# Kernel tuning notes

Hardware: AMD Instinct MI355X
Metric: run time of the kernel (lower is better)

The kernel has to match this reference:

```python
import jax, jax.numpy as jnp
import numpy as np

N_U, N_I, E = 500000, 50000, 1000000
H, C = 4, 32  # heads, per-head channels


def _seg_softmax(e, dst, n_dst):
    # e: [E, H] edge scores, softmax over edges sharing the same destination
    m = jax.ops.segment_max(e, dst, num_segments=n_dst)
    ex = jnp.exp(e - m[dst])
    s = jax.ops.segment_sum(ex, dst, num_segments=n_dst)
    return ex / (s[dst] + 1e-16)


def _gatv2(xl, xr, src, dst, att, bias, n_dst, edge_feat=None):
    # GATv2 bipartite message passing (PyG semantics, no self-loops for bipartite).
    # xl: [N_src,H,C] transformed source, xr: [N_dst,H,C] transformed destination
    h = xl[src] + xr[dst]                      # [E,H,C] gather + add
    if edge_feat is not None:
        h = h + edge_feat                      # [E,H,C]
    e = jnp.sum(jax.nn.leaky_relu(h, 0.2) * att, axis=-1)   # [E,H]
    alpha = _seg_softmax(e, dst, n_dst)                      # [E,H]
    out = jax.ops.segment_sum(alpha[..., None] * xl[src], dst, num_segments=n_dst)
    return out.reshape(n_dst, H * C) + bias    # concat heads + bias


def setup_inputs() -> dict:
    key = jax.random.key(0)
    ks = iter(jax.random.split(key, 32))
    p = lambda *s: jax.random.normal(next(ks), s, dtype=jnp.float32) * 0.05
    inp = {
        "customer_x": jax.random.normal(next(ks), (N_U, 101), dtype=jnp.float32),
        "fund_x": jax.random.normal(next(ks), (N_I, 1), dtype=jnp.float32),
        "edge_attr": jax.random.uniform(next(ks), (E, 3), dtype=jnp.float32),
        "edge_src": jax.random.randint(next(ks), (E,), 0, N_U),
        "edge_dst": jax.random.randint(next(ks), (E,), 0, N_I),
        # input projections
        "user_W": p(101, 32), "user_b": jnp.zeros((32,), jnp.float32),
        "item_W": p(1, 32),   "item_b": jnp.zeros((32,), jnp.float32),
        # conv1: GATv2Conv((32,32), 32, heads=4, edge_dim=3)
        "c1_Wl": p(32, H * C), "c1_bl": jnp.zeros((H * C,), jnp.float32),
        "c1_Wr": p(32, H * C), "c1_br": jnp.zeros((H * C,), jnp.float32),
        "c1_We": p(3, H * C),
        "c1_att": p(H, C), "c1_bias": jnp.zeros((H * C,), jnp.float32),
        # conv2: GATv2Conv((128,32), 32, heads=4), called without edge_attr
        "c2_Wl": p(H * C, H * C), "c2_bl": jnp.zeros((H * C,), jnp.float32),
        "c2_Wr": p(32, H * C),    "c2_br": jnp.zeros((H * C,), jnp.float32),
        "c2_att": p(H, C), "c2_bias": jnp.zeros((H * C,), jnp.float32),
        # classifier MLP: 128 -> 64 -> 1
        "cls_W1": p(128, 64), "cls_b1": jnp.zeros((64,), jnp.float32),
        "cls_W2": p(64, 1),   "cls_b2": jnp.zeros((1,), jnp.float32),
    }
    return inp


def reference(customer_x, fund_x, edge_attr, edge_src, edge_dst,
              user_W, user_b, item_W, item_b,
              c1_Wl, c1_bl, c1_Wr, c1_br, c1_We, c1_att, c1_bias,
              c2_Wl, c2_bl, c2_Wr, c2_br, c2_att, c2_bias,
              cls_W1, cls_b1, cls_W2, cls_b2):
    user_x = customer_x @ user_W + user_b            # [N_U,32]
    item_x = fund_x @ item_W + item_b                # [N_I,32]
    # conv1: customer -> fund (dst = fund)
    xl1 = (user_x @ c1_Wl + c1_bl).reshape(N_U, H, C)
    xr1 = (item_x @ c1_Wr + c1_br).reshape(N_I, H, C)
    ef1 = (edge_attr @ c1_We).reshape(E, H, C)
    item_h = jax.nn.relu(_gatv2(xl1, xr1, edge_src, edge_dst, c1_att, c1_bias, N_I, ef1))
    # conv2: fund -> customer (edge_index flipped, no edge_attr)
    xl2 = (item_h @ c2_Wl + c2_bl).reshape(N_I, H, C)
    xr2 = (user_x @ c2_Wr + c2_br).reshape(N_U, H, C)
    user_h = _gatv2(xl2, xr2, edge_dst, edge_src, c2_att, c2_bias, N_U)  # [N_U,128]
    # anomaly classifier
    hid = jax.nn.relu(user_h @ cls_W1 + cls_b1)
    scores = jax.nn.sigmoid(hid @ cls_W2 + cls_b2)   # [N_U,1]
    return scores
```

## Files before the change

kernel.cpp:

```cpp
#include <hip/hip_runtime.h>
#include <cstdint>
#include <cstddef>

#define NU 500000
#define NI 50000
#define NE 1000000
#define HC 128
#define NH 4

typedef __attribute__((ext_vector_type(8))) short bf16x8;
typedef __attribute__((ext_vector_type(4))) float f32x4;

union frag_u { bf16x8 v; unsigned int u[4]; };

__device__ __forceinline__ unsigned int pack_bf2(float x, float y) {
    unsigned int r;
    asm("v_cvt_pk_bf16_f32 %0, %1, %2" : "=v"(r) : "v"(x), "v"(y));
    return r;
}
__device__ __forceinline__ float2 unpack_bf2(unsigned int v) {
    return make_float2(__uint_as_float(v << 16),
                       __uint_as_float(v & 0xffff0000u));
}
__device__ __forceinline__ unsigned short pack_bf1(float x) {
    unsigned int b = __float_as_uint(x);
    b += 0x7fffu + ((b >> 16) & 1u);
    return (unsigned short)(b >> 16);
}

__device__ __forceinline__ float head_reduce(float p) {
    p += __shfl_xor(p, 8, 16);
    p += __shfl_xor(p, 4, 16);
    p += __shfl_xor(p, 2, 16);
    p += __shfl_xor(p, 1, 16);
    return p;
}

__global__ void wprep(const float* __restrict__ user_W, const float* __restrict__ user_b,
                      const float* __restrict__ c1_Wl, const float* __restrict__ c1_bl,
                      const float* __restrict__ c2_Wr, const float* __restrict__ c2_br,
                      const float* __restrict__ c2_Wl, unsigned short* __restrict__ Bp)
{
    const int t = blockIdx.x * 256 + threadIdx.x;
    const int mat = t >> 14;
    const int k = (t >> 7) & 127;
    const int n = t & 127;
    float val = 0.f;
    if (mat == 2) {
        val = c2_Wl[k * 128 + n];
    } else {
        const float* W2 = mat ? c2_Wr : c1_Wl;
        if (k < 101) {
            for (int q = 0; q < 32; ++q) val = fmaf(user_W[k * 32 + q], W2[q * 128 + n], val);
        } else if (k == 101) {
            for (int q = 0; q < 32; ++q) val = fmaf(user_b[q], W2[q * 128 + n], val);
            val += (mat ? c2_br : c1_bl)[n];
        }
    }
    const int fi = (mat * 8 + (n >> 4)) * 4 + (k >> 5);
    const int lane_ = (n & 15) + ((k >> 3) & 3) * 16;
    Bp[(size_t)fi * 512 + lane_ * 8 + (k & 7)] = pack_bf1(val);
}

__global__ void w1prep(const float* __restrict__ W1, unsigned short* __restrict__ Bp1)
{
    const int t = blockIdx.x * 256 + threadIdx.x;
    const int k = t >> 6;
    const int n = t & 63;
    const float val = W1[k * 64 + n];
    const int fi = (n >> 4) * 4 + (k >> 5);
    const int lane_ = (n & 15) + ((k >> 3) & 3) * 16;
    Bp1[(size_t)fi * 512 + lane_ * 8 + (k & 7)] = pack_bf1(val);
}

__global__ void wvbb_prep(const float* __restrict__ item_W, const float* __restrict__ item_b,
                          const float* __restrict__ c1_Wr, const float* __restrict__ c1_br,
                          float* __restrict__ wvbb)
{
    const int j = threadIdx.x;
    if (j >= 128) return;
    float wv = 0.f, bb = 0.f;
    for (int q = 0; q < 32; ++q) {
        wv = fmaf(item_W[q], c1_Wr[q * 128 + j], wv);
        bb = fmaf(item_b[q], c1_Wr[q * 128 + j], bb);
    }
    wvbb[j] = wv;
    wvbb[128 + j] = bb + c1_br[j];
}

__global__ __launch_bounds__(256)
void mfma_user(const float* __restrict__ cx, const unsigned short* __restrict__ Bp,
               unsigned short* __restrict__ outL, unsigned short* __restrict__ outR, int M)
{
    __shared__ float xs[64 * 108];

    const int tid = threadIdx.x;
    const int lane = tid & 63;
    const int wid = tid >> 6;
    const int rowblk = blockIdx.x * 64;
    const int rows = min(64, M - rowblk);

    const float* src = cx + (size_t)rowblk * 101;
    const int total = rows * 101;
    for (int i = tid; i < total; i += 256) {
        const int r = i / 101;
        const int c = i - r * 101;
        xs[r * 108 + c] = src[i];
    }
    __syncthreads();

    const int rowbase = wid * 16;
    if (rowbase >= rows) return;
    const int row = lane & 15;
    const int chunk = lane >> 4;
    const float* rowp = xs + (rowbase + row) * 108;

    frag_u a[4];
    #pragma unroll
    for (int ks = 0; ks < 3; ++ks) {
        const int kb = ks * 32 + chunk * 8;
        const float4 p = *(const float4*)(rowp + kb);
        const float4 q = *(const float4*)(rowp + kb + 4);
        a[ks].u[0] = pack_bf2(p.x, p.y);
        a[ks].u[1] = pack_bf2(p.z, p.w);
        a[ks].u[2] = pack_bf2(q.x, q.y);
        a[ks].u[3] = pack_bf2(q.z, q.w);
    }
    {
        float v0 = 0.f, v1 = 0.f, v2 = 0.f, v3 = 0.f, v4 = 0.f, v5 = 0.f;
        if (chunk == 0) {
            const float4 p = *(const float4*)(rowp + 96);
            v0 = p.x; v1 = p.y; v2 = p.z; v3 = p.w;
            v4 = rowp[100];
            v5 = 1.0f;
        }
        a[3].u[0] = pack_bf2(v0, v1);
        a[3].u[1] = pack_bf2(v2, v3);
        a[3].u[2] = pack_bf2(v4, v5);
        a[3].u[3] = 0u;
    }

    unsigned short* xpo = (unsigned short*)(xs + (size_t)wid * 16 * 108);

    const bf16x8* bfr = (const bf16x8*)Bp;
    #pragma unroll
    for (int mat = 0; mat < 2; ++mat) {
        unsigned short* outp = mat ? outR : outL;
        #pragma unroll
        for (int nf = 0; nf < 8; ++nf) {
            f32x4 acc = {0.f, 0.f, 0.f, 0.f};
            const int fi = (mat * 8 + nf) * 4;
            acc = __builtin_amdgcn_mfma_f32_16x16x32_bf16(a[0].v, bfr[(fi + 0) * 64 + lane], acc, 0, 0, 0);
            acc = __builtin_amdgcn_mfma_f32_16x16x32_bf16(a[1].v, bfr[(fi + 1) * 64 + lane], acc, 0, 0, 0);
            acc = __builtin_amdgcn_mfma_f32_16x16x32_bf16(a[2].v, bfr[(fi + 2) * 64 + lane], acc, 0, 0, 0);
            acc = __builtin_amdgcn_mfma_f32_16x16x32_bf16(a[3].v, bfr[(fi + 3) * 64 + lane], acc, 0, 0, 0);
            const int col = nf * 16 + row;
            #pragma unroll
            for (int j = 0; j < 4; ++j)
                xpo[(chunk * 4 + j) * 140 + col] = pack_bf1(acc[j]);
        }
        #pragma unroll
        for (int i = 0; i < 4; ++i) {
            const int r = i * 4 + chunk;
            const bf16x8 v = *(const bf16x8*)&xpo[r * 140 + row * 8];
            *(bf16x8*)(outp + (size_t)(rowblk + rowbase + r) * 128 + row * 8) = v;
        }
    }
}

__global__ __launch_bounds__(256)
void mfma_xl2(const float* __restrict__ X, const unsigned short* __restrict__ Bp,
              const float* __restrict__ bias, unsigned short* __restrict__ outp, int M)
{
    const int lane = threadIdx.x & 63;
    const int wt = (blockIdx.x * blockDim.x + threadIdx.x) >> 6;
    const int rowbase = wt * 16;
    if (rowbase >= M) return;
    const int chunk = lane >> 4;
    const float* rowp = X + (size_t)(rowbase + (lane & 15)) * 128;

    frag_u a[4];
    #pragma unroll
    for (int ks = 0; ks < 4; ++ks) {
        const int kb = ks * 32 + chunk * 8;
        const float4 p = *(const float4*)(rowp + kb);
        const float4 q = *(const float4*)(rowp + kb + 4);
        a[ks].u[0] = pack_bf2(p.x, p.y);
        a[ks].u[1] = pack_bf2(p.z, p.w);
        a[ks].u[2] = pack_bf2(q.x, q.y);
        a[ks].u[3] = pack_bf2(q.z, q.w);
    }

    const bf16x8* bfr = (const bf16x8*)Bp;
    #pragma unroll
    for (int nf = 0; nf < 8; ++nf) {
        f32x4 acc = {0.f, 0.f, 0.f, 0.f};
        const int fi = (16 + nf) * 4;
        acc = __builtin_amdgcn_mfma_f32_16x16x32_bf16(a[0].v, bfr[(fi + 0) * 64 + lane], acc, 0, 0, 0);
        acc = __builtin_amdgcn_mfma_f32_16x16x32_bf16(a[1].v, bfr[(fi + 1) * 64 + lane], acc, 0, 0, 0);
        acc = __builtin_amdgcn_mfma_f32_16x16x32_bf16(a[2].v, bfr[(fi + 2) * 64 + lane], acc, 0, 0, 0);
        acc = __builtin_amdgcn_mfma_f32_16x16x32_bf16(a[3].v, bfr[(fi + 3) * 64 + lane], acc, 0, 0, 0);
        const int col = nf * 16 + (lane & 15);
        const float bv = bias[col];
        #pragma unroll
        for (int j = 0; j < 4; ++j)
            outp[(size_t)(rowbase + chunk * 4 + j) * 128 + col] = pack_bf1(acc[j] + bv);
    }
}

__global__ void hist_rank(const int* __restrict__ src, const int* __restrict__ dst,
                          int* __restrict__ cntU, int* __restrict__ cntI,
                          int* __restrict__ rankU, int* __restrict__ rankI, int E)
{
    for (int i = blockIdx.x * blockDim.x + threadIdx.x; i < E;
         i += gridDim.x * blockDim.x) {
        rankU[i] = atomicAdd(&cntU[src[i]], 1);
        rankI[i] = atomicAdd(&cntI[dst[i]], 1);
    }
}

__global__ void scan_blocks(const int* __restrict__ in, int* __restrict__ out,
                            int* __restrict__ blockSums, int n)
{
    __shared__ int lds[256];
    const int tid = threadIdx.x;
    const int base = blockIdx.x * 1024 + tid * 4;
    int v[4];
    #pragma unroll
    for (int j = 0; j < 4; ++j) { int idx = base + j; v[j] = (idx < n) ? in[idx] : 0; }
    int t = v[0] + v[1] + v[2] + v[3];
    lds[tid] = t;
    __syncthreads();
    for (int off = 1; off < 256; off <<= 1) {
        int x = (tid >= off) ? lds[tid - off] : 0;
        __syncthreads();
        lds[tid] += x;
        __syncthreads();
    }
    int excl = lds[tid] - t;
    if (tid == 255 && blockSums) blockSums[blockIdx.x] = lds[255];
    int run = excl;
    #pragma unroll
    for (int j = 0; j < 4; ++j) {
        int idx = base + j;
        if (idx < n) out[idx] = run;
        run += v[j];
    }
}

__global__ void scan_add(int* __restrict__ out, const int* __restrict__ bss, int n)
{
    const int add = bss[blockIdx.x];
    const int base = blockIdx.x * 1024 + threadIdx.x * 4;
    #pragma unroll
    for (int j = 0; j < 4; ++j) { int idx = base + j; if (idx < n) out[idx] += add; }
}

__global__ void scatter_ranked(const int* __restrict__ src, const int* __restrict__ dst,
                               const float* __restrict__ eattr,
                               const int* __restrict__ offU, const int* __restrict__ offI,
                               const int* __restrict__ rankU, const int* __restrict__ rankI,
                               int* __restrict__ sFund, uint4* __restrict__ sE1, int E)
{
    for (int i = blockIdx.x * blockDim.x + threadIdx.x; i < E;
         i += gridDim.x * blockDim.x) {
        const int s = src[i];
        const int d = dst[i];
        const float a0 = eattr[3 * (size_t)i];
        const float a1 = eattr[3 * (size_t)i + 1];
        const float a2 = eattr[3 * (size_t)i + 2];
        const int p1 = offI[d] + rankI[i];
        const int p2 = offU[s] + rankU[i];
        sE1[p1] = make_uint4((unsigned int)s, __float_as_uint(a0),
                             __float_as_uint(a1), __float_as_uint(a2));
        sFund[p2] = d;
    }
}

__device__ __forceinline__ void conv1_edge(uint4 e, unsigned int vbits, float2 vr,
                                           float2 av, float2 w0, float2 w1, float2 w2,
                                           float& acc0, float& acc1, float& s)
{
    const float2 vl = unpack_bf2(vbits);
    const float e0 = __uint_as_float(e.y);
    const float e1 = __uint_as_float(e.z);
    const float e2 = __uint_as_float(e.w);
    float h0 = vl.x + vr.x + e0 * w0.x + e1 * w1.x + e2 * w2.x;
    float h1 = vl.y + vr.y + e0 * w0.y + e1 * w1.y + e2 * w2.y;
    h0 = h0 > 0.f ? h0 : 0.2f * h0;
    h1 = h1 > 0.f ? h1 : 0.2f * h1;
    const float p = head_reduce(h0 * av.x + h1 * av.y);
    const float ex = __expf(p);
    acc0 = fmaf(ex, vl.x, acc0);
    acc1 = fmaf(ex, vl.y, acc1);
    s += ex;
}

__global__ void conv1_fused(const unsigned int* __restrict__ xl,
                            const float* __restrict__ fund_x,
                            const float* __restrict__ wvbb,
                            const int* __restrict__ offI, const int* __restrict__ cnt,
                            const uint4* __restrict__ sE,
                            const float* __restrict__ We, const float* __restrict__ att,
                            const float* __restrict__ bias,
                            float* __restrict__ outF, int ndst)
{
    const int tid = threadIdx.x;
    const int lane = tid & 63;
    const int wid = tid >> 6;
    const int d = blockIdx.x * 4 + wid;
    if (d >= ndst) return;

    const int ch = lane * 2;
    const float2 av = *(const float2*)(att + ch);
    const float2 w0 = *(const float2*)(We + ch);
    const float2 w1 = *(const float2*)(We + HC + ch);
    const float2 w2 = *(const float2*)(We + 2 * HC + ch);
    const float2 bv = *(const float2*)(bias + ch);

    const float fx = fund_x[d];
    const float2 wv = *(const float2*)(wvbb + ch);
    const float2 bb = *(const float2*)(wvbb + 128 + ch);
    const float2 vr = make_float2(fmaf(fx, wv.x, bb.x), fmaf(fx, wv.y, bb.y));

    const int start = offI[d];
    const int end = start + cnt[d];

    float acc0 = 0.f, acc1 = 0.f, s = 0.f;
    int pos = start;
    for (; pos + 8 <= end; pos += 8) {
        uint4 e[8];
        unsigned int v[8];
        #pragma unroll
        for (int j = 0; j < 8; ++j) e[j] = sE[pos + j];
        #pragma unroll
        for (int j = 0; j < 8; ++j) v[j] = xl[(size_t)e[j].x * 64 + lane];
        #pragma unroll
        for (int j = 0; j < 8; ++j)
            conv1_edge(e[j], v[j], vr, av, w0, w1, w2, acc0, acc1, s);
    }
    for (; pos + 4 <= end; pos += 4) {
        uint4 e[4];
        unsigned int v[4];
        #pragma unroll
        for (int j = 0; j < 4; ++j) e[j] = sE[pos + j];
        #pragma unroll
        for (int j = 0; j < 4; ++j) v[j] = xl[(size_t)e[j].x * 64 + lane];
        #pragma unroll
        for (int j = 0; j < 4; ++j)
            conv1_edge(e[j], v[j], vr, av, w0, w1, w2, acc0, acc1, s);
    }
    for (; pos < end; ++pos) {
        const uint4 e = sE[pos];
        const unsigned int v = xl[(size_t)e.x * 64 + lane];
        conv1_edge(e, v, vr, av, w0, w1, w2, acc0, acc1, s);
    }
    const float inv = 1.f / (s + 1e-16f);
    const float o0 = fmaxf(acc0 * inv + bv.x, 0.f);
    const float o1 = fmaxf(acc1 * inv + bv.y, 0.f);
    *(float2*)(outF + (size_t)d * HC + ch) = make_float2(o0, o1);
}

__device__ __forceinline__ void conv2_edge(unsigned int vbits, float2 vr, float2 av,
                                           float& acc0, float& acc1, float& s)
{
    const float2 vl = unpack_bf2(vbits);
    float h0 = vl.x + vr.x;
    float h1 = vl.y + vr.y;
    h0 = h0 > 0.f ? h0 : 0.2f * h0;
    h1 = h1 > 0.f ? h1 : 0.2f * h1;
    const float p = head_reduce(h0 * av.x + h1 * av.y);
    const float ex = __expf(p);
    acc0 = fmaf(ex, vl.x, acc0);
    acc1 = fmaf(ex, vl.y, acc1);
    s += ex;
}

__global__ __launch_bounds__(256)
void conv2_cls(const unsigned int* __restrict__ xl2,
               const unsigned int* __restrict__ xr2,
               const int* __restrict__ offU, const int* __restrict__ cnt,
               const int* __restrict__ sFund,
               const float* __restrict__ att, const float* __restrict__ cbias,
               const unsigned short* __restrict__ Bp1,
               const float* __restrict__ b1, const float* __restrict__ W2,
               const float* __restrict__ b2,
               float* __restrict__ out, int nusr)
{
    __shared__ unsigned short xs[4][16][136];

    const int lane = threadIdx.x & 63;
    const int wid = threadIdx.x >> 6;
    const int wt = (blockIdx.x * blockDim.x + threadIdx.x) >> 6;
    const int u0 = wt * 16;
    if (u0 >= nusr) return;

    const int ch = lane * 2;
    const float2 av = *(const float2*)(att + ch);
    const float2 bv = *(const float2*)(cbias + ch);

    int so = 0, ctv = 0;
    if (lane < 16) {
        so = offU[u0 + lane];
        ctv = cnt[u0 + lane];
    }
    const int eo = so + ctv;
    const int S = __builtin_amdgcn_readlane(so, 0);
    const int E = __builtin_amdgcn_readlane(eo, 15);

    int u = 0;
    int end_u = __builtin_amdgcn_readlane(eo, 0);
    unsigned int vrb_next = xr2[(size_t)(u0 + 1) * 64 + lane];
    float2 vr = unpack_bf2(xr2[(size_t)u0 * 64 + lane]);
    float acc0 = 0.f, acc1 = 0.f, s = 0.f;

    #define FINALIZE() {                                                        \
        const float inv = 1.f / (s + 1e-16f);                                   \
        *(unsigned int*)&xs[wid][u][ch] = pack_bf2(acc0 * inv + bv.x,           \
                                                   acc1 * inv + bv.y);          \
        acc0 = acc1 = s = 0.f;                                                  \
        ++u;                                                                    \
        if (u < 16) {                                                           \
            end_u = __builtin_amdgcn_readlane(eo, u);                           \
            vr = unpack_bf2(vrb_next);                                          \
            if (u + 1 < 16) vrb_next = xr2[(size_t)(u0 + u + 1) * 64 + lane];   \
        }                                                                       \
    }

    int pos = S;
    while (pos < E) {
        const int f0 = sFund[pos];
        const int f1 = (pos + 1 < E) ? sFund[pos + 1] : f0;
        const int f2 = (pos + 2 < E) ? sFund[pos + 2] : f0;
        const int f3 = (pos + 3 < E) ? sFund[pos + 3] : f0;
        const unsigned int v0 = xl2[(size_t)f0 * 64 + lane];
        const unsigned int v1 = xl2[(size_t)f1 * 64 + lane];
        const unsigned int v2 = xl2[(size_t)f2 * 64 + lane];
        const unsigned int v3 = xl2[(size_t)f3 * 64 + lane];

        while (pos == end_u) FINALIZE();
        conv2_edge(v0, vr, av, acc0, acc1, s);
        if (pos + 1 < E) {
            while (pos + 1 == end_u) FINALIZE();
            conv2_edge(v1, vr, av, acc0, acc1, s);
        }
        if (pos + 2 < E) {
            while (pos + 2 == end_u) FINALIZE();
            conv2_edge(v2, vr, av, acc0, acc1, s);
        }
        if (pos + 3 < E) {
            while (pos + 3 == end_u) FINALIZE();
            conv2_edge(v3, vr, av, acc0, acc1, s);
        }
        pos += 4;
    }
    while (u < 16) FINALIZE();
    #undef FINALIZE

    const int row = lane & 15;
    const int chunk = lane >> 4;
    bf16x8 a[4];
    #pragma unroll
    for (int ks = 0; ks < 4; ++ks)
        a[ks] = *(const bf16x8*)&xs[wid][row][ks * 32 + chunk * 8];

    const bf16x8* bfr = (const bf16x8*)Bp1;
    float racc[4] = {0.f, 0.f, 0.f, 0.f};
    #pragma unroll
    for (int g = 0; g < 4; ++g) {
        f32x4 acc = {0.f, 0.f, 0.f, 0.f};
        const int fi = g * 4;
        acc = __builtin_amdgcn_mfma_f32_16x16x32_bf16(a[0], bfr[(fi + 0) * 64 + lane], acc, 0, 0, 0);
        acc = __builtin_amdgcn_mfma_f32_16x16x32_bf16(a[1], bfr[(fi + 1) * 64 + lane], acc, 0, 0, 0);
        acc = __builtin_amdgcn_mfma_f32_16x16x32_bf16(a[2], bfr[(fi + 2) * 64 + lane], acc, 0, 0, 0);
        acc = __builtin_amdgcn_mfma_f32_16x16x32_bf16(a[3], bfr[(fi + 3) * 64 + lane], acc, 0, 0, 0);
        const int col = g * 16 + row;
        const float b1v = b1[col];
        const float w2v = W2[col];
        #pragma unroll
        for (int j = 0; j < 4; ++j)
            racc[j] = fmaf(fmaxf(acc[j] + b1v, 0.f), w2v, racc[j]);
    }
    #pragma unroll
    for (int j = 0; j < 4; ++j) {
        racc[j] += __shfl_xor(racc[j], 1, 16);
        racc[j] += __shfl_xor(racc[j], 2, 16);
        racc[j] += __shfl_xor(racc[j], 4, 16);
        racc[j] += __shfl_xor(racc[j], 8, 16);
    }
    if (row == 0) {
        const float b2v = b2[0];
        #pragma unroll
        for (int j = 0; j < 4; ++j) {
            const int r = u0 + chunk * 4 + j;
            if (r < nusr) out[r] = 1.f / (1.f + expf(-(racc[j] + b2v)));
        }
    }
}

extern "C" void kernel_launch(void* const* d_in, const int* in_sizes, int n_in,
                              void* d_out, int out_size, void* d_ws, size_t ws_size,
                              hipStream_t stream)
{
    const float* customer_x = (const float*)d_in[0];
    const float* fund_x     = (const float*)d_in[1];
    const float* edge_attr  = (const float*)d_in[2];
    const int*   edge_src   = (const int*)d_in[3];
    const int*   edge_dst   = (const int*)d_in[4];
    const float* user_W = (const float*)d_in[5];
    const float* user_b = (const float*)d_in[6];
    const float* item_W = (const float*)d_in[7];
    const float* item_b = (const float*)d_in[8];
    const float* c1_Wl  = (const float*)d_in[9];
    const float* c1_bl  = (const float*)d_in[10];
    const float* c1_Wr  = (const float*)d_in[11];
    const float* c1_br  = (const float*)d_in[12];
    const float* c1_We  = (const float*)d_in[13];
    const float* c1_att = (const float*)d_in[14];
    const float* c1_bias= (const float*)d_in[15];
    const float* c2_Wl  = (const float*)d_in[16];
    const float* c2_bl  = (const float*)d_in[17];
    const float* c2_Wr  = (const float*)d_in[18];
    const float* c2_br  = (const float*)d_in[19];
    const float* c2_att = (const float*)d_in[20];
    const float* c2_bias= (const float*)d_in[21];
    const float* cls_W1 = (const float*)d_in[22];
    const float* cls_b1 = (const float*)d_in[23];
    const float* cls_W2 = (const float*)d_in[24];
    const float* cls_b2 = (const float*)d_in[25];
    float* out = (float*)d_out;

    float* ws = (float*)d_ws;
    size_t off = 0;
    unsigned short* B1 = (unsigned short*)(ws + off); off += (size_t)NU * 64;
    unsigned short* B2 = (unsigned short*)(ws + off); off += (size_t)NU * 64;
    float* F = ws + off; off += (size_t)NI * HC;
    unsigned short* G = (unsigned short*)(ws + off); off += (size_t)NI * 64;
    int* cnt1  = (int*)(ws + off); off += NI;
    int* off1  = (int*)(ws + off); off += NI;
    int* cnt2  = (int*)(ws + off); off += NU;
    int* off2  = (int*)(ws + off); off += NU;
    int* bs    = (int*)(ws + off); off += 1024;
    int* bss   = (int*)(ws + off); off += 1024;
    uint4* sE1 = (uint4*)(ws + off); off += (size_t)NE * 4;
    int* sFund = (int*)(ws + off); off += NE;
    int* rankU = (int*)(ws + off); off += NE;
    int* rankI = (int*)(ws + off); off += NE;
    unsigned short* Bp = (unsigned short*)(ws + off); off += 12288 + 256;
    unsigned short* Bp1 = (unsigned short*)(ws + off); off += 4096 + 256;
    float* wvbb = ws + off; off += 256;

    hipMemsetAsync(cnt1, 0, NI * sizeof(int), stream);
    hipMemsetAsync(cnt2, 0, NU * sizeof(int), stream);

    hist_rank<<<1024, 256, 0, stream>>>(edge_src, edge_dst, cnt2, cnt1,
                                        rankU, rankI, NE);
    const int nb1 = (NI + 1023) / 1024;
    const int nb2 = (NU + 1023) / 1024;
    scan_blocks<<<nb1, 256, 0, stream>>>(cnt1, off1, bs, NI);
    scan_blocks<<<1,   256, 0, stream>>>(bs, bss, nullptr, nb1);
    scan_add<<<nb1, 256, 0, stream>>>(off1, bss, NI);
    scan_blocks<<<nb2, 256, 0, stream>>>(cnt2, off2, bs, NU);
    scan_blocks<<<1,   256, 0, stream>>>(bs, bss, nullptr, nb2);
    scan_add<<<nb2, 256, 0, stream>>>(off2, bss, NU);
    scatter_ranked<<<2048, 256, 0, stream>>>(edge_src, edge_dst, edge_attr,
                                             off2, off1, rankU, rankI,
                                             sFund, sE1, NE);

    wprep<<<192, 256, 0, stream>>>(user_W, user_b, c1_Wl, c1_bl,
                                   c2_Wr, c2_br, c2_Wl, Bp);
    w1prep<<<32, 256, 0, stream>>>(cls_W1, Bp1);
    wvbb_prep<<<1, 128, 0, stream>>>(item_W, item_b, c1_Wr, c1_br, wvbb);

    mfma_user<<<(NU + 63) / 64, 256, 0, stream>>>(customer_x, Bp, B1, B2, NU);

    conv1_fused<<<NI / 4, 256, 0, stream>>>((const unsigned int*)B1, fund_x, wvbb,
                                            off1, cnt1, sE1,
                                            c1_We, c1_att, c1_bias, F, NI);

    mfma_xl2<<<(NI / 16 + 3) / 4, 256, 0, stream>>>(F, Bp, c2_bl, G, NI);

    const int waves2 = (NU + 15) / 16;
    conv2_cls<<<(waves2 + 3) / 4, 256, 0, stream>>>(
        (const unsigned int*)G, (const unsigned int*)B2, off2, cnt2, sFund,
        c2_att, c2_bias, Bp1, cls_b1, cls_W2, cls_b2, out, NU);
}
```

Measured before the change: 537.3 us.

## Fuse edge scatter into user MFMA kernel via extra blocks for overlap

Removes the standalone scatter_ranked launch and appends 2048 extra blocks to the user-projection MFMA kernel, which perform the edge scatter. The aim is to overlap the memory-bound scatter with the projection and save one kernel launch and drain. In exchange, the scatter blocks are scheduled after the projection blocks, so overlap may be limited and both parts compete for memory bandwidth. The combined kernel also keeps the 27 KB LDS allocation for the scatter blocks, which can lower occupancy for them.

```diff
diff --git a/kernel.cpp b/kernel.cpp
--- a/kernel.cpp
+++ b/kernel.cpp
@@ -89,10 +89,33 @@
 }
 
 __global__ __launch_bounds__(256)
-void mfma_user(const float* __restrict__ cx, const unsigned short* __restrict__ Bp,
-               unsigned short* __restrict__ outL, unsigned short* __restrict__ outR, int M)
+void mfma_user_scatter(const float* __restrict__ cx, const unsigned short* __restrict__ Bp,
+                       unsigned short* __restrict__ outL, unsigned short* __restrict__ outR,
+                       int M, int nub,
+                       const int* __restrict__ src, const int* __restrict__ dst,
+                       const float* __restrict__ eattr,
+                       const int* __restrict__ offU, const int* __restrict__ offI,
+                       const int* __restrict__ rankU, const int* __restrict__ rankI,
+                       int* __restrict__ sFund, uint4* __restrict__ sE1, int E, int nscat)
 {
     __shared__ float xs[64 * 108];
+
+    if (blockIdx.x >= nub) {
+        const int bid = blockIdx.x - nub;
+        for (int i = bid * 256 + threadIdx.x; i < E; i += nscat * 256) {
+            const int s = src[i];
+            const int d = dst[i];
+            const float a0 = eattr[3 * (size_t)i];
+            const float a1 = eattr[3 * (size_t)i + 1];
+            const float a2 = eattr[3 * (size_t)i + 2];
+            const int p1 = offI[d] + rankI[i];
+            const int p2 = offU[s] + rankU[i];
+            sE1[p1] = make_uint4((unsigned int)s, __float_as_uint(a0),
+                                 __float_as_uint(a1), __float_as_uint(a2));
+            sFund[p2] = d;
+        }
+        return;
+    }
 
     const int tid = threadIdx.x;
     const int lane = tid & 63;
@@ -100,12 +123,12 @@
     const int rowblk = blockIdx.x * 64;
     const int rows = min(64, M - rowblk);
 
-    const float* src = cx + (size_t)rowblk * 101;
+    const float* srcp = cx + (size_t)rowblk * 101;
     const int total = rows * 101;
     for (int i = tid; i < total; i += 256) {
         const int r = i / 101;
         const int c = i - r * 101;
-        xs[r * 108 + c] = src[i];
+        xs[r * 108 + c] = srcp[i];
     }
     __syncthreads();
 
@@ -254,27 +277,6 @@
     const int base = blockIdx.x * 1024 + threadIdx.x * 4;
     #pragma unroll
     for (int j = 0; j < 4; ++j) { int idx = base + j; if (idx < n) out[idx] += add; }
-}
-
-__global__ void scatter_ranked(const int* __restrict__ src, const int* __restrict__ dst,
-                               const float* __restrict__ eattr,
-                               const int* __restrict__ offU, const int* __restrict__ offI,
-                               const int* __restrict__ rankU, const int* __restrict__ rankI,
-                               int* __restrict__ sFund, uint4* __restrict__ sE1, int E)
-{
-    for (int i = blockIdx.x * blockDim.x + threadIdx.x; i < E;
-         i += gridDim.x * blockDim.x) {
-        const int s = src[i];
-        const int d = dst[i];
-        const float a0 = eattr[3 * (size_t)i];
-        const float a1 = eattr[3 * (size_t)i + 1];
-        const float a2 = eattr[3 * (size_t)i + 2];
-        const int p1 = offI[d] + rankI[i];
-        const int p2 = offU[s] + rankU[i];
-        sE1[p1] = make_uint4((unsigned int)s, __float_as_uint(a0),
-                             __float_as_uint(a1), __float_as_uint(a2));
-        sFund[p2] = d;
-    }
 }
 
 __device__ __forceinline__ void conv1_edge(uint4 e, unsigned int vbits, float2 vr,
@@ -563,16 +565,18 @@
     scan_blocks<<<nb2, 256, 0, stream>>>(cnt2, off2, bs, NU);
     scan_blocks<<<1,   256, 0, stream>>>(bs, bss, nullptr, nb2);
     scan_add<<<nb2, 256, 0, stream>>>(off2, bss, NU);
-    scatter_ranked<<<2048, 256, 0, stream>>>(edge_src, edge_dst, edge_attr,
-                                             off2, off1, rankU, rankI,
-                                             sFund, sE1, NE);
 
     wprep<<<192, 256, 0, stream>>>(user_W, user_b, c1_Wl, c1_bl,
                                    c2_Wr, c2_br, c2_Wl, Bp);
     w1prep<<<32, 256, 0, stream>>>(cls_W1, Bp1);
     wvbb_prep<<<1, 128, 0, stream>>>(item_W, item_b, c1_Wr, c1_br, wvbb);
 
-    mfma_user<<<(NU + 63) / 64, 256, 0, stream>>>(customer_x, Bp, B1, B2, NU);
+    const int nub = (NU + 63) / 64;
+    const int nscat = 2048;
+    mfma_user_scatter<<<nub + nscat, 256, 0, stream>>>(
+        customer_x, Bp, B1, B2, NU, nub,
+        edge_src, edge_dst, edge_attr, off2, off1, rankU, rankI,
+        sFund, sE1, NE, nscat);
 
     conv1_fused<<<NI / 4, 256, 0, stream>>>((const unsigned int*)B1, fund_x, wvbb,
                                             off1, cnt1, sE1,
```

After: 535.3 us. Within noise of the previous version (-0.4%).
